# Optimization experiments

Measured on AMD Instinct MI355X. Metric: run time of the kernel, lower is better.

The kernel has to match this reference:

```python
import jax, jax.numpy as jnp
import numpy as np

B, S, D_IN, D_OUT = 4, 2048, 4096, 4096


def setup_inputs() -> dict:
    key = jax.random.key(0)
    k_x, k_w, k_s, k_b = jax.random.split(key, 4)
    x = jax.random.normal(k_x, (B, S, D_IN), dtype=jnp.float32)
    # simulated int8 compressed weight, values in [-128, 127]
    weight_int8 = jax.random.randint(k_w, (D_OUT, D_IN), 0, 255, dtype=jnp.int32) - 128
    # per-output-row dequant scale (positive)
    scale = jax.random.uniform(k_s, (D_OUT,), dtype=jnp.float32) * 0.01 + 1e-4
    bias = jax.random.normal(k_b, (D_OUT,), dtype=jnp.float32)
    return {"x": x, "weight_int8": weight_int8, "scale": scale, "bias": bias}


def reference(x, weight_int8, scale, bias):
    # dequantize: int8 -> fp, per-row scale, reshape to (out, in)
    weight_fp = weight_int8.astype(x.dtype) * scale[:, None]  # [D_OUT, D_IN]
    # F.linear: x @ W^T + b
    out = jnp.einsum("bsd,od->bso", x, weight_fp) + bias
    return out
```

## Files before the change

### kernel.cpp

```cpp
#include <hip/hip_runtime.h>


#define BM 256
#define BN 256
#define BKB 128

constexpr int Mdim = 8192;
constexpr int Ndim = 4096;
constexpr int Kdim = 4096;
constexpr int KT = Kdim / BKB;

typedef __attribute__((ext_vector_type(4)))  int   int32x4;
typedef __attribute__((ext_vector_type(16))) int   int32x16;
typedef __attribute__((ext_vector_type(8)))  short short8;
typedef __attribute__((ext_vector_type(4)))  float f32x4;
typedef unsigned short ushort_t;

__device__ __forceinline__ unsigned short f2bf(float f) {
    union { float f; unsigned u; } v; v.f = f;
    unsigned r = v.u + 0x7FFFu + ((v.u >> 16) & 1u);
    return (unsigned short)(r >> 16);
}

__device__ __forceinline__ void gload_lds16(const void* g, void* l) {
    __builtin_amdgcn_global_load_lds(
        (const __attribute__((address_space(1))) void*)g,
        (__attribute__((address_space(3))) void*)l, 16, 0, 0);
}

#define BARRIER() __builtin_amdgcn_s_barrier()
#define LGKM0()   asm volatile("s_waitcnt lgkmcnt(0)" ::: "memory")
#define WAITV0()  asm volatile("s_waitcnt vmcnt(0)" ::: "memory")
#define WAITV6()  asm volatile("s_waitcnt vmcnt(6)" ::: "memory")

#define MFMAQ(MH, NH) do {                                                   \
    __builtin_amdgcn_s_setprio(1);                                           \
    _Pragma("unroll") for (int mt = 0; mt < 2; ++mt)                         \
    _Pragma("unroll") for (int ks = 0; ks < 4; ++ks)                         \
        acc[(MH)*2+mt][NH] = __builtin_amdgcn_mfma_i32_32x32x32_i8(          \
            af[mt][ks], bf[NH][ks], acc[(MH)*2+mt][NH], 0, 0, 0);            \
    __builtin_amdgcn_s_setprio(0);                                           \
} while (0)


__global__ __launch_bounds__(256)
void quant_x_rowwise(const float* __restrict__ x, char* __restrict__ xq,
                     float* __restrict__ sx) {
    const int row = blockIdx.x;
    const float4* xr = reinterpret_cast<const float4*>(x + (size_t)row * Kdim);
    const int tid = threadIdx.x;
    float4 v[4];
    float am = 0.f;
    #pragma unroll
    for (int j = 0; j < 4; ++j) {
        v[j] = xr[tid + 256 * j];
        am = fmaxf(am, fmaxf(fmaxf(fabsf(v[j].x), fabsf(v[j].y)),
                             fmaxf(fabsf(v[j].z), fabsf(v[j].w))));
    }
    #pragma unroll
    for (int off = 32; off; off >>= 1)
        am = fmaxf(am, __shfl_xor(am, off, 64));
    __shared__ float red[4];
    if ((tid & 63) == 0) red[tid >> 6] = am;
    __syncthreads();
    am = fmaxf(fmaxf(red[0], red[1]), fmaxf(red[2], red[3]));
    am = fmaxf(am, 1e-30f);
    if (tid == 0) sx[row] = am / 127.f;
    const float inv = 127.f / am;
    int* outw = reinterpret_cast<int*>(xq + (size_t)row * Kdim);
    #pragma unroll
    for (int j = 0; j < 4; ++j) {
        const int q0 = (int)rintf(v[j].x * inv) & 255;
        const int q1 = (int)rintf(v[j].y * inv) & 255;
        const int q2 = (int)rintf(v[j].z * inv) & 255;
        const int q3 = (int)rintf(v[j].w * inv) & 255;
        outw[tid + 256 * j] = q0 | (q1 << 8) | (q2 << 16) | (q3 << 24);
    }
}

__global__ __launch_bounds__(256)
void pack_w_int8(const int* __restrict__ w, char* __restrict__ wq, int n4) {
    int idx = blockIdx.x * blockDim.x + threadIdx.x;
    const int stride = gridDim.x * blockDim.x;
    int* out = reinterpret_cast<int*>(wq);
    for (int i = idx; i < n4; i += stride) {
        const int4 a = reinterpret_cast<const int4*>(w)[i];
        out[i] = (a.x & 255) | ((a.y & 255) << 8) |
                 ((a.z & 255) << 16) | ((a.w & 255) << 24);
    }
}


__global__ __launch_bounds__(512, 2)
void gemm_i8_8phase(const char* __restrict__ A,
                    const char* __restrict__ B,
                    const float* __restrict__ scale,
                    const float* __restrict__ bias,
                    const float* __restrict__ sx,
                    float* __restrict__ Out)
{
    __shared__ __align__(16) char smem[2][4][16384];

    const int tid = threadIdx.x;
    int bid = blockIdx.x;
    bid = (bid & 7) * 64 + (bid >> 3);
    const int tn = bid & 15;
    const int tm = bid >> 4;
    const int brow = tm * BM;
    const int bcol = tn * BN;

    const int lane = tid & 63;
    const int w    = tid >> 6;
    const int wr   = w >> 2;
    const int wc   = w & 3;
    const int r32  = lane & 31;
    const int h    = lane >> 5;
    const size_t K1 = (size_t)Kdim;

    const int swzb = ((lane & 7) ^ (lane >> 3) ^ (w & 3)) << 4;
    const char* aStageSrc = A + (size_t)(brow + w * 8 + (lane >> 3)) * K1 + swzb;
    const char* bStageSrc = B + (size_t)(bcol + w * 8 + (lane >> 3)) * K1 + swzb;

    auto stageA = [&](int bufb, int hh, int tt) {
        const char* s = aStageSrc + (size_t)(hh * 128) * K1 + (size_t)tt * BKB;
        char* d = &smem[bufb][hh][w * 1024];
        gload_lds16(s, d);
        gload_lds16(s + 64 * K1, d + 8192);
    };
    auto stageB = [&](int bufb, int hh, int tt) {
        const char* s = bStageSrc + (size_t)(hh * 128) * K1 + (size_t)tt * BKB;
        char* d = &smem[bufb][2 + hh][w * 1024];
        gload_lds16(s, d);
        gload_lds16(s + 64 * K1, d + 8192);
    };

    const char* aBase[2] = { &smem[0][wr][0] + r32 * 128,
                             &smem[1][wr][0] + r32 * 128 };
    const char* bBase[2] = { &smem[0][2 + (wc >> 1)][0] + ((wc & 1) * 64 + r32) * 128,
                             &smem[1][2 + (wc >> 1)][0] + ((wc & 1) * 64 + r32) * 128 };
    const int frx = ((r32 & 7) ^ (r32 >> 3)) << 4;
    int colb[4];
    #pragma unroll
    for (int ks = 0; ks < 4; ++ks) colb[ks] = (ks * 32 + h * 16) ^ frx;

    int32x16 acc[4][2] = {};
    int32x4 af[2][4], bf[2][4];

    auto ldA = [&](const char* base, int MH) {
        #pragma unroll
        for (int mt = 0; mt < 2; ++mt) {
            const char* p = base + ((MH) * 2 + mt) * 4096;
            #pragma unroll
            for (int ks = 0; ks < 4; ++ks)
                af[mt][ks] = *reinterpret_cast<const int32x4*>(p + colb[ks]);
        }
    };
    auto ldB = [&](const char* base) {
        #pragma unroll
        for (int nt = 0; nt < 2; ++nt) {
            const char* p = base + nt * 4096;
            #pragma unroll
            for (int ks = 0; ks < 4; ++ks)
                bf[nt][ks] = *reinterpret_cast<const int32x4*>(p + colb[ks]);
        }
    };

    stageB(0, 0, 0); stageB(0, 1, 0); stageA(0, 0, 0); stageA(0, 1, 0);
    stageB(1, 0, 1); stageB(1, 1, 1); stageA(1, 0, 1);
    WAITV6();
    BARRIER();

    for (int i = 0; i < KT / 2 - 1; ++i) {
        const int t = 2 * i;

        ldB(bBase[0]); ldA(aBase[0], 0);
        stageA(1, 1, t + 1);
        BARRIER(); LGKM0();
        MFMAQ(0, 0);
        BARRIER();
        stageB(0, 0, t + 2);
        BARRIER(); LGKM0();
        MFMAQ(0, 1);
        BARRIER();
        ldA(aBase[0], 1);
        stageB(0, 1, t + 2);
        BARRIER(); LGKM0();
        MFMAQ(1, 0);
        BARRIER();
        stageA(0, 0, t + 2);
        BARRIER(); LGKM0();
        MFMAQ(1, 1);
        WAITV6();
        BARRIER();
        ldB(bBase[1]); ldA(aBase[1], 0);
        stageA(0, 1, t + 2);
        BARRIER(); LGKM0();
        MFMAQ(0, 0);
        BARRIER();
        stageB(1, 0, t + 3);
        BARRIER(); LGKM0();
        MFMAQ(0, 1);
        BARRIER();
        ldA(aBase[1], 1);
        stageB(1, 1, t + 3);
        BARRIER(); LGKM0();
        MFMAQ(1, 0);
        BARRIER();
        stageA(1, 0, t + 3);
        BARRIER(); LGKM0();
        MFMAQ(1, 1);
        WAITV6();
        BARRIER();
    }

    {
        ldB(bBase[0]); ldA(aBase[0], 0);
        stageA(1, 1, KT - 1);
        BARRIER(); LGKM0();
        MFMAQ(0, 0);
        BARRIER();
        MFMAQ(0, 1);
        BARRIER();
        ldA(aBase[0], 1);
        BARRIER(); LGKM0();
        MFMAQ(1, 0);
        BARRIER();
        MFMAQ(1, 1);
        WAITV0();
        BARRIER();
        ldB(bBase[1]); ldA(aBase[1], 0);
        BARRIER(); LGKM0();
        MFMAQ(0, 0);
        MFMAQ(0, 1);
        ldA(aBase[1], 1);
        LGKM0();
        MFMAQ(1, 0);
        MFMAQ(1, 1);
    }

    #pragma unroll
    for (int nt = 0; nt < 2; ++nt) {
        const int col = bcol + wc * 64 + nt * 32 + r32;
        const float sc = scale[col];
        const float bi = bias[col];
        #pragma unroll
        for (int mt = 0; mt < 4; ++mt) {
            const int rb = brow + wr * 128 + mt * 32 + 4 * h;
            #pragma unroll
            for (int q = 0; q < 4; ++q) {
                const int r4 = rb + 8 * q;
                #pragma unroll
                for (int r = 0; r < 4; ++r) {
                    const float sxr = sx[r4 + r];
                    Out[(size_t)(r4 + r) * Ndim + col] =
                        (float)acc[mt][nt][q * 4 + r] * (sc * sxr) + bi;
                }
            }
        }
    }
}


__device__ __forceinline__ int swz_fb(int row, int colbyte) {
    return row * 128 + (colbyte ^ ((row & 7) << 4));
}

__global__ __launch_bounds__(256)
void compressed_linear_fb(const float* __restrict__ X,
                          const int*   __restrict__ W,
                          const float* __restrict__ scale,
                          const float* __restrict__ bias,
                          float* __restrict__ Out)
{
    __shared__ __align__(16) ushort_t lA[128 * 64];
    __shared__ __align__(16) ushort_t lB[128 * 64];
    const int tid = threadIdx.x;
    const int bid = blockIdx.x;
    const int tn = bid & 31, tm = bid >> 5;
    const int brow = tm * 128, bcol = tn * 128;
    const int r0 = tid >> 3, c0 = tid & 7;
    float4 aPre[4][2]; int4 bPre[4][2];
    const int lane = tid & 63, w = tid >> 6;
    const int wr = w >> 1, wc = w & 1, fr = lane & 15, fq = lane >> 4;
    f32x4 acc[4][4] = {};

    auto loadTiles = [&](int t) {
        const int k0 = t * 64;
        #pragma unroll
        for (int i = 0; i < 4; i++) {
            const int row = r0 + 32 * i;
            const float4* pa = reinterpret_cast<const float4*>(X + (size_t)(brow + row) * Kdim + k0 + c0 * 8);
            aPre[i][0] = pa[0]; aPre[i][1] = pa[1];
            const int4* pb = reinterpret_cast<const int4*>(W + (size_t)(bcol + row) * Kdim + k0 + c0 * 8);
            bPre[i][0] = pb[0]; bPre[i][1] = pb[1];
        }
    };
    auto writeLDS = [&]() {
        #pragma unroll
        for (int i = 0; i < 4; i++) {
            const int row = r0 + 32 * i;
            const int off = swz_fb(row, c0 * 16);
            short8 va, vb;
            va[0] = (short)f2bf(aPre[i][0].x); va[1] = (short)f2bf(aPre[i][0].y);
            va[2] = (short)f2bf(aPre[i][0].z); va[3] = (short)f2bf(aPre[i][0].w);
            va[4] = (short)f2bf(aPre[i][1].x); va[5] = (short)f2bf(aPre[i][1].y);
            va[6] = (short)f2bf(aPre[i][1].z); va[7] = (short)f2bf(aPre[i][1].w);
            vb[0] = (short)f2bf((float)bPre[i][0].x); vb[1] = (short)f2bf((float)bPre[i][0].y);
            vb[2] = (short)f2bf((float)bPre[i][0].z); vb[3] = (short)f2bf((float)bPre[i][0].w);
            vb[4] = (short)f2bf((float)bPre[i][1].x); vb[5] = (short)f2bf((float)bPre[i][1].y);
            vb[6] = (short)f2bf((float)bPre[i][1].z); vb[7] = (short)f2bf((float)bPre[i][1].w);
            *reinterpret_cast<short8*>(reinterpret_cast<char*>(lA) + off) = va;
            *reinterpret_cast<short8*>(reinterpret_cast<char*>(lB) + off) = vb;
        }
    };

    loadTiles(0);
    for (int t = 0; t < Kdim / 64; t++) {
        writeLDS();
        __syncthreads();
        if (t + 1 < Kdim / 64) loadTiles(t + 1);
        #pragma unroll
        for (int kk = 0; kk < 2; kk++) {
            short8 afv[4], bfv[4];
            const int cb = kk * 64 + fq * 16;
            #pragma unroll
            for (int m = 0; m < 4; m++) {
                const int row = wr * 64 + m * 16 + fr;
                afv[m] = *reinterpret_cast<const short8*>(reinterpret_cast<const char*>(lA) + swz_fb(row, cb));
            }
            #pragma unroll
            for (int n = 0; n < 4; n++) {
                const int row = wc * 64 + n * 16 + fr;
                bfv[n] = *reinterpret_cast<const short8*>(reinterpret_cast<const char*>(lB) + swz_fb(row, cb));
            }
            #pragma unroll
            for (int m = 0; m < 4; m++)
                #pragma unroll
                for (int n = 0; n < 4; n++)
                    acc[m][n] = __builtin_amdgcn_mfma_f32_16x16x32_bf16(afv[m], bfv[n], acc[m][n], 0, 0, 0);
        }
        __syncthreads();
    }
    #pragma unroll
    for (int n = 0; n < 4; n++) {
        const int col = bcol + wc * 64 + n * 16 + fr;
        const float sc = scale[col];
        const float bi = bias[col];
        #pragma unroll
        for (int m = 0; m < 4; m++) {
            const int rbase = brow + wr * 64 + m * 16 + fq * 4;
            #pragma unroll
            for (int j = 0; j < 4; j++)
                Out[(size_t)(rbase + j) * Ndim + col] = acc[m][n][j] * sc + bi;
        }
    }
}


extern "C" void kernel_launch(void* const* d_in, const int* in_sizes, int n_in,
                              void* d_out, int out_size, void* d_ws, size_t ws_size,
                              hipStream_t stream) {
    const float* x     = (const float*)d_in[0];
    const int*   w8    = (const int*)d_in[1];
    const float* scale = (const float*)d_in[2];
    const float* bias  = (const float*)d_in[3];
    float* out = (float*)d_out;

    const size_t xq_bytes = (size_t)Mdim * Kdim;
    const size_t wq_bytes = (size_t)Ndim * Kdim;
    const size_t sx_bytes = (size_t)Mdim * sizeof(float);

    if (ws_size >= xq_bytes + wq_bytes + sx_bytes) {
        char*  xq = (char*)d_ws;
        char*  wq = (char*)d_ws + xq_bytes;
        float* sx = (float*)((char*)d_ws + xq_bytes + wq_bytes);
        quant_x_rowwise<<<Mdim, 256, 0, stream>>>(x, xq, sx);
        pack_w_int8<<<2048, 256, 0, stream>>>(w8, wq, (Ndim * Kdim) / 4);
        dim3 grid((Mdim / BM) * (Ndim / BN));
        gemm_i8_8phase<<<grid, dim3(512), 0, stream>>>(xq, wq, scale, bias, sx, out);
    } else {
        dim3 grid((Mdim / 128) * (Ndim / 128));
        compressed_linear_fb<<<grid, dim3(256), 0, stream>>>(x, w8, scale, bias, out);
    }
}
```

Before: 194.2 us.

## Shrink int8 GEMM tile to 128x128 with 4 waves and restructured staging

Replaces the 256x256 tile, 8-wave int8 MFMA GEMM with a 128x128 tile, 4-wave kernel. Each K-step is staged into LDS as a whole tile per buffer instead of in half-tile pieces, and the interleaving of LDS fragment loads and global-to-LDS stages within the phase loop is reworked. Smaller tiles give more blocks and less LDS per block, which may raise occupancy. In exchange, arithmetic intensity per block drops and global and L2 traffic for A and B roughly doubles.

```diff
diff --git a/kernel.cpp b/kernel.cpp
--- a/kernel.cpp
+++ b/kernel.cpp
@@ -1,8 +1,8 @@
 #include <hip/hip_runtime.h>
 
 
-#define BM 256
-#define BN 256
+#define BM 128
+#define BN 128
 #define BKB 128
 
 constexpr int Mdim = 8192;
@@ -31,14 +31,13 @@
 #define BARRIER() __builtin_amdgcn_s_barrier()
 #define LGKM0()   asm volatile("s_waitcnt lgkmcnt(0)" ::: "memory")
 #define WAITV0()  asm volatile("s_waitcnt vmcnt(0)" ::: "memory")
-#define WAITV6()  asm volatile("s_waitcnt vmcnt(6)" ::: "memory")
-
-#define MFMAQ(MH, NH) do {                                                   \
+#define WAITV8()  asm volatile("s_waitcnt vmcnt(8)" ::: "memory")
+
+#define MFMAQ(MT, NT) do {                                                   \
     __builtin_amdgcn_s_setprio(1);                                           \
-    _Pragma("unroll") for (int mt = 0; mt < 2; ++mt)                         \
     _Pragma("unroll") for (int ks = 0; ks < 4; ++ks)                         \
-        acc[(MH)*2+mt][NH] = __builtin_amdgcn_mfma_i32_32x32x32_i8(          \
-            af[mt][ks], bf[NH][ks], acc[(MH)*2+mt][NH], 0, 0, 0);            \
+        acc[MT][NT] = __builtin_amdgcn_mfma_i32_32x32x32_i8(                 \
+            af[MT][ks], bf[NT][ks], acc[MT][NT], 0, 0, 0);                   \
     __builtin_amdgcn_s_setprio(0);                                           \
 } while (0)
 
@@ -91,28 +90,28 @@
 }
 
 
-__global__ __launch_bounds__(512, 2)
-void gemm_i8_8phase(const char* __restrict__ A,
-                    const char* __restrict__ B,
-                    const float* __restrict__ scale,
-                    const float* __restrict__ bias,
-                    const float* __restrict__ sx,
-                    float* __restrict__ Out)
+__global__ __launch_bounds__(256, 2)
+void gemm_i8_128(const char* __restrict__ A,
+                 const char* __restrict__ B,
+                 const float* __restrict__ scale,
+                 const float* __restrict__ bias,
+                 const float* __restrict__ sx,
+                 float* __restrict__ Out)
 {
-    __shared__ __align__(16) char smem[2][4][16384];
+    __shared__ __align__(16) char smem[2][2][16384];
 
     const int tid = threadIdx.x;
     int bid = blockIdx.x;
-    bid = (bid & 7) * 64 + (bid >> 3);
-    const int tn = bid & 15;
-    const int tm = bid >> 4;
+    bid = (bid & 7) * 256 + (bid >> 3);
+    const int tn = bid & 31;
+    const int tm = bid >> 5;
     const int brow = tm * BM;
     const int bcol = tn * BN;
 
     const int lane = tid & 63;
     const int w    = tid >> 6;
-    const int wr   = w >> 2;
-    const int wc   = w & 3;
+    const int wr   = w >> 1;
+    const int wc   = w & 1;
     const int r32  = lane & 31;
     const int h    = lane >> 5;
     const size_t K1 = (size_t)Kdim;
@@ -121,104 +120,97 @@
     const char* aStageSrc = A + (size_t)(brow + w * 8 + (lane >> 3)) * K1 + swzb;
     const char* bStageSrc = B + (size_t)(bcol + w * 8 + (lane >> 3)) * K1 + swzb;
 
-    auto stageA = [&](int bufb, int hh, int tt) {
-        const char* s = aStageSrc + (size_t)(hh * 128) * K1 + (size_t)tt * BKB;
-        char* d = &smem[bufb][hh][w * 1024];
-        gload_lds16(s, d);
-        gload_lds16(s + 64 * K1, d + 8192);
-    };
-    auto stageB = [&](int bufb, int hh, int tt) {
-        const char* s = bStageSrc + (size_t)(hh * 128) * K1 + (size_t)tt * BKB;
-        char* d = &smem[bufb][2 + hh][w * 1024];
-        gload_lds16(s, d);
-        gload_lds16(s + 64 * K1, d + 8192);
-    };
-
-    const char* aBase[2] = { &smem[0][wr][0] + r32 * 128,
-                             &smem[1][wr][0] + r32 * 128 };
-    const char* bBase[2] = { &smem[0][2 + (wc >> 1)][0] + ((wc & 1) * 64 + r32) * 128,
-                             &smem[1][2 + (wc >> 1)][0] + ((wc & 1) * 64 + r32) * 128 };
+    auto stageA = [&](int bufb, int tt) {
+        const char* s = aStageSrc + (size_t)tt * BKB;
+        char* d = &smem[bufb][0][w * 1024];
+        #pragma unroll
+        for (int i = 0; i < 4; ++i)
+            gload_lds16(s + (size_t)(32 * i) * K1, d + i * 4096);
+    };
+    auto stageB = [&](int bufb, int tt) {
+        const char* s = bStageSrc + (size_t)tt * BKB;
+        char* d = &smem[bufb][1][w * 1024];
+        #pragma unroll
+        for (int i = 0; i < 4; ++i)
+            gload_lds16(s + (size_t)(32 * i) * K1, d + i * 4096);
+    };
+
+    const char* aBase[2] = { &smem[0][0][0] + (wr * 64 + r32) * 128,
+                             &smem[1][0][0] + (wr * 64 + r32) * 128 };
+    const char* bBase[2] = { &smem[0][1][0] + (wc * 64 + r32) * 128,
+                             &smem[1][1][0] + (wc * 64 + r32) * 128 };
     const int frx = ((r32 & 7) ^ (r32 >> 3)) << 4;
     int colb[4];
     #pragma unroll
     for (int ks = 0; ks < 4; ++ks) colb[ks] = (ks * 32 + h * 16) ^ frx;
 
-    int32x16 acc[4][2] = {};
+    int32x16 acc[2][2] = {};
     int32x4 af[2][4], bf[2][4];
 
-    auto ldA = [&](const char* base, int MH) {
-        #pragma unroll
-        for (int mt = 0; mt < 2; ++mt) {
-            const char* p = base + ((MH) * 2 + mt) * 4096;
-            #pragma unroll
-            for (int ks = 0; ks < 4; ++ks)
-                af[mt][ks] = *reinterpret_cast<const int32x4*>(p + colb[ks]);
-        }
-    };
-    auto ldB = [&](const char* base) {
-        #pragma unroll
-        for (int nt = 0; nt < 2; ++nt) {
-            const char* p = base + nt * 4096;
-            #pragma unroll
-            for (int ks = 0; ks < 4; ++ks)
-                bf[nt][ks] = *reinterpret_cast<const int32x4*>(p + colb[ks]);
-        }
-    };
-
-    stageB(0, 0, 0); stageB(0, 1, 0); stageA(0, 0, 0); stageA(0, 1, 0);
-    stageB(1, 0, 1); stageB(1, 1, 1); stageA(1, 0, 1);
-    WAITV6();
+    auto ldA = [&](const char* base, int mt) {
+        #pragma unroll
+        for (int ks = 0; ks < 4; ++ks)
+            af[mt][ks] = *reinterpret_cast<const int32x4*>(base + mt * 4096 + colb[ks]);
+    };
+    auto ldB = [&](const char* base, int nt) {
+        #pragma unroll
+        for (int ks = 0; ks < 4; ++ks)
+            bf[nt][ks] = *reinterpret_cast<const int32x4*>(base + nt * 4096 + colb[ks]);
+    };
+
+    stageB(0, 0); stageA(0, 0);
+    stageB(1, 1); stageA(1, 1);
+    WAITV8();
     BARRIER();
 
     for (int i = 0; i < KT / 2 - 1; ++i) {
         const int t = 2 * i;
 
-        ldB(bBase[0]); ldA(aBase[0], 0);
-        stageA(1, 1, t + 1);
+        ldA(aBase[0], 0); ldB(bBase[0], 0);
         BARRIER(); LGKM0();
         MFMAQ(0, 0);
         BARRIER();
-        stageB(0, 0, t + 2);
+        ldB(bBase[0], 1);
         BARRIER(); LGKM0();
         MFMAQ(0, 1);
         BARRIER();
         ldA(aBase[0], 1);
-        stageB(0, 1, t + 2);
+        stageB(0, t + 2);
         BARRIER(); LGKM0();
         MFMAQ(1, 0);
         BARRIER();
-        stageA(0, 0, t + 2);
+        stageA(0, t + 2);
         BARRIER(); LGKM0();
         MFMAQ(1, 1);
-        WAITV6();
-        BARRIER();
-        ldB(bBase[1]); ldA(aBase[1], 0);
-        stageA(0, 1, t + 2);
+        WAITV8();
+        BARRIER();
+        ldA(aBase[1], 0); ldB(bBase[1], 0);
         BARRIER(); LGKM0();
         MFMAQ(0, 0);
         BARRIER();
-        stageB(1, 0, t + 3);
+        ldB(bBase[1], 1);
         BARRIER(); LGKM0();
         MFMAQ(0, 1);
         BARRIER();
         ldA(aBase[1], 1);
-        stageB(1, 1, t + 3);
+        stageB(1, t + 3);
         BARRIER(); LGKM0();
         MFMAQ(1, 0);
         BARRIER();
-        stageA(1, 0, t + 3);
+        stageA(1, t + 3);
         BARRIER(); LGKM0();
         MFMAQ(1, 1);
-        WAITV6();
+        WAITV8();
         BARRIER();
     }
 
     {
-        ldB(bBase[0]); ldA(aBase[0], 0);
-        stageA(1, 1, KT - 1);
+        ldA(aBase[0], 0); ldB(bBase[0], 0);
         BARRIER(); LGKM0();
         MFMAQ(0, 0);
         BARRIER();
+        ldB(bBase[0], 1);
+        BARRIER(); LGKM0();
         MFMAQ(0, 1);
         BARRIER();
         ldA(aBase[0], 1);
@@ -228,9 +220,11 @@
         MFMAQ(1, 1);
         WAITV0();
         BARRIER();
-        ldB(bBase[1]); ldA(aBase[1], 0);
-        BARRIER(); LGKM0();
+        ldA(aBase[1], 0); ldB(bBase[1], 0);
+        LGKM0();
         MFMAQ(0, 0);
+        ldB(bBase[1], 1);
+        LGKM0();
         MFMAQ(0, 1);
         ldA(aBase[1], 1);
         LGKM0();
@@ -244,8 +238,8 @@
         const float sc = scale[col];
         const float bi = bias[col];
         #pragma unroll
-        for (int mt = 0; mt < 4; ++mt) {
-            const int rb = brow + wr * 128 + mt * 32 + 4 * h;
+        for (int mt = 0; mt < 2; ++mt) {
+            const int rb = brow + wr * 64 + mt * 32 + 4 * h;
             #pragma unroll
             for (int q = 0; q < 4; ++q) {
                 const int r4 = rb + 8 * q;
@@ -377,7 +371,7 @@
         quant_x_rowwise<<<Mdim, 256, 0, stream>>>(x, xq, sx);
         pack_w_int8<<<2048, 256, 0, stream>>>(w8, wq, (Ndim * Kdim) / 4);
         dim3 grid((Mdim / BM) * (Ndim / BN));
-        gemm_i8_8phase<<<grid, dim3(512), 0, stream>>>(xq, wq, scale, bias, sx, out);
+        gemm_i8_128<<<grid, dim3(256), 0, stream>>>(xq, wq, scale, bias, sx, out);
     } else {
         dim3 grid((Mdim / 128) * (Ndim / 128));
         compressed_linear_fb<<<grid, dim3(256), 0, stream>>>(x, w8, scale, bias, out);
```

Result: slower. 223.9 us (+15.3%).

## Replace eight-phase interleaved GEMM schedule with two-cluster flat pipeline

Applied to the files above, without the earlier changes.

Restructures the int8 MFMA main loop. The old schedule split each K-tile into four small MFMA quadrants, each wrapped in barriers and explicit LDS waits; the new one runs two larger MFMA clusters per K-tile, covering both N halves at once. All global-to-LDS staging for a future tile is issued between the two clusters, and the vmcnt threshold changes to match the new issue order. The aim is to cut barrier and waitcnt overhead and give the MFMA units longer uninterrupted runs. The cost is coarser interleaving of memory traffic with compute, and more in-flight loads bunched together.

```diff
diff --git a/kernel.cpp b/kernel.cpp
--- a/kernel.cpp
+++ b/kernel.cpp
@@ -29,16 +29,16 @@
 }
 
 #define BARRIER() __builtin_amdgcn_s_barrier()
-#define LGKM0()   asm volatile("s_waitcnt lgkmcnt(0)" ::: "memory")
 #define WAITV0()  asm volatile("s_waitcnt vmcnt(0)" ::: "memory")
-#define WAITV6()  asm volatile("s_waitcnt vmcnt(6)" ::: "memory")
-
-#define MFMAQ(MH, NH) do {                                                   \
+#define WAITV4()  asm volatile("s_waitcnt vmcnt(4)" ::: "memory")
+
+#define CLUSTER(MBASE) do {                                                  \
     __builtin_amdgcn_s_setprio(1);                                           \
     _Pragma("unroll") for (int mt = 0; mt < 2; ++mt)                         \
+    _Pragma("unroll") for (int nt = 0; nt < 2; ++nt)                         \
     _Pragma("unroll") for (int ks = 0; ks < 4; ++ks)                         \
-        acc[(MH)*2+mt][NH] = __builtin_amdgcn_mfma_i32_32x32x32_i8(          \
-            af[mt][ks], bf[NH][ks], acc[(MH)*2+mt][NH], 0, 0, 0);            \
+        acc[(MBASE)+mt][nt] = __builtin_amdgcn_mfma_i32_32x32x32_i8(         \
+            af[mt][ks], bf[nt][ks], acc[(MBASE)+mt][nt], 0, 0, 0);           \
     __builtin_amdgcn_s_setprio(0);                                           \
 } while (0)
 
@@ -92,12 +92,12 @@
 
 
 __global__ __launch_bounds__(512, 2)
-void gemm_i8_8phase(const char* __restrict__ A,
-                    const char* __restrict__ B,
-                    const float* __restrict__ scale,
-                    const float* __restrict__ bias,
-                    const float* __restrict__ sx,
-                    float* __restrict__ Out)
+void gemm_i8_flat(const char* __restrict__ A,
+                  const char* __restrict__ B,
+                  const float* __restrict__ scale,
+                  const float* __restrict__ bias,
+                  const float* __restrict__ sx,
+                  float* __restrict__ Out)
 {
     __shared__ __align__(16) char smem[2][4][16384];
 
@@ -165,77 +165,52 @@
         }
     };
 
-    stageB(0, 0, 0); stageB(0, 1, 0); stageA(0, 0, 0); stageA(0, 1, 0);
-    stageB(1, 0, 1); stageB(1, 1, 1); stageA(1, 0, 1);
-    WAITV6();
+    stageA(0, 0, 0); stageA(0, 1, 0);
+    stageB(0, 0, 0); stageB(0, 1, 0);
+    stageB(1, 0, 1); stageB(1, 1, 1);
+    WAITV4();
     BARRIER();
 
     for (int i = 0; i < KT / 2 - 1; ++i) {
         const int t = 2 * i;
 
         ldB(bBase[0]); ldA(aBase[0], 0);
-        stageA(1, 1, t + 1);
-        BARRIER(); LGKM0();
-        MFMAQ(0, 0);
-        BARRIER();
-        stageB(0, 0, t + 2);
-        BARRIER(); LGKM0();
-        MFMAQ(0, 1);
-        BARRIER();
+        BARRIER();
+        CLUSTER(0);
         ldA(aBase[0], 1);
-        stageB(0, 1, t + 2);
-        BARRIER(); LGKM0();
-        MFMAQ(1, 0);
-        BARRIER();
-        stageA(0, 0, t + 2);
-        BARRIER(); LGKM0();
-        MFMAQ(1, 1);
-        WAITV6();
-        BARRIER();
+        stageA(1, 0, t + 1); stageA(1, 1, t + 1);
+        stageB(0, 0, t + 2); stageB(0, 1, t + 2);
+        CLUSTER(2);
+        WAITV4();
+        BARRIER();
+
         ldB(bBase[1]); ldA(aBase[1], 0);
-        stageA(0, 1, t + 2);
-        BARRIER(); LGKM0();
-        MFMAQ(0, 0);
-        BARRIER();
-        stageB(1, 0, t + 3);
-        BARRIER(); LGKM0();
-        MFMAQ(0, 1);
-        BARRIER();
+        BARRIER();
+        CLUSTER(0);
         ldA(aBase[1], 1);
-        stageB(1, 1, t + 3);
-        BARRIER(); LGKM0();
-        MFMAQ(1, 0);
-        BARRIER();
-        stageA(1, 0, t + 3);
-        BARRIER(); LGKM0();
-        MFMAQ(1, 1);
-        WAITV6();
+        stageA(0, 0, t + 2); stageA(0, 1, t + 2);
+        stageB(1, 0, t + 3); stageB(1, 1, t + 3);
+        CLUSTER(2);
+        WAITV4();
         BARRIER();
     }
 
     {
         ldB(bBase[0]); ldA(aBase[0], 0);
-        stageA(1, 1, KT - 1);
-        BARRIER(); LGKM0();
-        MFMAQ(0, 0);
-        BARRIER();
-        MFMAQ(0, 1);
-        BARRIER();
+        BARRIER();
+        CLUSTER(0);
         ldA(aBase[0], 1);
-        BARRIER(); LGKM0();
-        MFMAQ(1, 0);
-        BARRIER();
-        MFMAQ(1, 1);
+        stageA(1, 0, KT - 1); stageA(1, 1, KT - 1);
+        CLUSTER(2);
         WAITV0();
         BARRIER();
+    }
+    {
         ldB(bBase[1]); ldA(aBase[1], 0);
-        BARRIER(); LGKM0();
-        MFMAQ(0, 0);
-        MFMAQ(0, 1);
+        BARRIER();
+        CLUSTER(0);
         ldA(aBase[1], 1);
-        LGKM0();
-        MFMAQ(1, 0);
-        MFMAQ(1, 1);
+        CLUSTER(2);
     }
 
     #pragma unroll
@@ -377,7 +352,7 @@
         quant_x_rowwise<<<Mdim, 256, 0, stream>>>(x, xq, sx);
         pack_w_int8<<<2048, 256, 0, stream>>>(w8, wq, (Ndim * Kdim) / 4);
         dim3 grid((Mdim / BM) * (Ndim / BN));
-        gemm_i8_8phase<<<grid, dim3(512), 0, stream>>>(xq, wq, scale, bias, sx, out);
+        gemm_i8_flat<<<grid, dim3(512), 0, stream>>>(xq, wq, scale, bias, sx, out);
     } else {
         dim3 grid((Mdim / 128) * (Ndim / 128));
         compressed_linear_fb<<<grid, dim3(256), 0, stream>>>(x, w8, scale, bias, out);
```

New measurement: 194.5 us. No clear change (+0.2%).

## Software-pipeline LDS fragment loads with MFMA using split A register buffers

Applied to the files above, without the earlier changes.

Restructures the int8 GEMM main loop so LDS reads of the next fragments (A high half, next-buffer B and A low half) are issued while MFMAs on the current fragments execute. A fragments are split into separate Lo/Hi register sets, and the loop drops to one barrier per phase instead of two. The vmcnt wait is tightened so stage arrival is checked earlier. The extra live fragment registers raise register pressure at two blocks per CU, and the reordered barriers need the LDS buffer reuse to stay race-free.

```diff
diff --git a/kernel.cpp b/kernel.cpp
--- a/kernel.cpp
+++ b/kernel.cpp
@@ -31,14 +31,15 @@
 #define BARRIER() __builtin_amdgcn_s_barrier()
 #define LGKM0()   asm volatile("s_waitcnt lgkmcnt(0)" ::: "memory")
 #define WAITV0()  asm volatile("s_waitcnt vmcnt(0)" ::: "memory")
+#define WAITV4()  asm volatile("s_waitcnt vmcnt(4)" ::: "memory")
 #define WAITV6()  asm volatile("s_waitcnt vmcnt(6)" ::: "memory")
 
-#define MFMAQ(MH, NH) do {                                                   \
+#define MFMAC(AF, MB, NH) do {                                               \
     __builtin_amdgcn_s_setprio(1);                                           \
     _Pragma("unroll") for (int mt = 0; mt < 2; ++mt)                         \
     _Pragma("unroll") for (int ks = 0; ks < 4; ++ks)                         \
-        acc[(MH)*2+mt][NH] = __builtin_amdgcn_mfma_i32_32x32x32_i8(          \
-            af[mt][ks], bf[NH][ks], acc[(MH)*2+mt][NH], 0, 0, 0);            \
+        acc[(MB)+mt][NH] = __builtin_amdgcn_mfma_i32_32x32x32_i8(            \
+            AF[mt][ks], bf[NH][ks], acc[(MB)+mt][NH], 0, 0, 0);              \
     __builtin_amdgcn_s_setprio(0);                                           \
 } while (0)
 
@@ -92,12 +93,12 @@
 
 
 __global__ __launch_bounds__(512, 2)
-void gemm_i8_8phase(const char* __restrict__ A,
-                    const char* __restrict__ B,
-                    const float* __restrict__ scale,
-                    const float* __restrict__ bias,
-                    const float* __restrict__ sx,
-                    float* __restrict__ Out)
+void gemm_i8_pl(const char* __restrict__ A,
+                const char* __restrict__ B,
+                const float* __restrict__ scale,
+                const float* __restrict__ bias,
+                const float* __restrict__ sx,
+                float* __restrict__ Out)
 {
     __shared__ __align__(16) char smem[2][4][16384];
 
@@ -144,98 +145,98 @@
     for (int ks = 0; ks < 4; ++ks) colb[ks] = (ks * 32 + h * 16) ^ frx;
 
     int32x16 acc[4][2] = {};
-    int32x4 af[2][4], bf[2][4];
-
-    auto ldA = [&](const char* base, int MH) {
-        #pragma unroll
-        for (int mt = 0; mt < 2; ++mt) {
-            const char* p = base + ((MH) * 2 + mt) * 4096;
+    int32x4 afLo[2][4], afHi[2][4], bf[2][4];
+
+    auto ldB = [&](const char* base) {
+        #pragma unroll
+        for (int nt = 0; nt < 2; ++nt)
             #pragma unroll
             for (int ks = 0; ks < 4; ++ks)
-                af[mt][ks] = *reinterpret_cast<const int32x4*>(p + colb[ks]);
-        }
-    };
-    auto ldB = [&](const char* base) {
-        #pragma unroll
-        for (int nt = 0; nt < 2; ++nt) {
-            const char* p = base + nt * 4096;
+                bf[nt][ks] = *reinterpret_cast<const int32x4*>(base + nt * 4096 + colb[ks]);
+    };
+    auto ldALo = [&](const char* base) {
+        #pragma unroll
+        for (int mt = 0; mt < 2; ++mt)
             #pragma unroll
             for (int ks = 0; ks < 4; ++ks)
-                bf[nt][ks] = *reinterpret_cast<const int32x4*>(p + colb[ks]);
-        }
+                afLo[mt][ks] = *reinterpret_cast<const int32x4*>(base + mt * 4096 + colb[ks]);
+    };
+    auto ldAHi = [&](const char* base) {
+        #pragma unroll
+        for (int mt = 0; mt < 2; ++mt)
+            #pragma unroll
+            for (int ks = 0; ks < 4; ++ks)
+                afHi[mt][ks] = *reinterpret_cast<const int32x4*>(base + (2 + mt) * 4096 + colb[ks]);
     };
 
     stageB(0, 0, 0); stageB(0, 1, 0); stageA(0, 0, 0); stageA(0, 1, 0);
     stageB(1, 0, 1); stageB(1, 1, 1); stageA(1, 0, 1);
     WAITV6();
     BARRIER();
+    ldB(bBase[0]);
+    ldALo(aBase[0]);
+    BARRIER();
 
     for (int i = 0; i < KT / 2 - 1; ++i) {
         const int t = 2 * i;
 
-        ldB(bBase[0]); ldA(aBase[0], 0);
+        MFMAC(afLo, 0, 0);
+        ldAHi(aBase[0]);
         stageA(1, 1, t + 1);
-        BARRIER(); LGKM0();
-        MFMAQ(0, 0);
-        BARRIER();
+        LGKM0();
+        BARRIER();
+        MFMAC(afLo, 0, 1);
         stageB(0, 0, t + 2);
-        BARRIER(); LGKM0();
-        MFMAQ(0, 1);
-        BARRIER();
-        ldA(aBase[0], 1);
+        BARRIER();
+        MFMAC(afHi, 2, 0);
         stageB(0, 1, t + 2);
-        BARRIER(); LGKM0();
-        MFMAQ(1, 0);
-        BARRIER();
+        LGKM0();
+        WAITV4();
+        BARRIER();
+        MFMAC(afHi, 2, 1);
+        ldB(bBase[1]);
+        ldALo(aBase[1]);
         stageA(0, 0, t + 2);
-        BARRIER(); LGKM0();
-        MFMAQ(1, 1);
-        WAITV6();
-        BARRIER();
-        ldB(bBase[1]); ldA(aBase[1], 0);
+        BARRIER();
+        MFMAC(afLo, 0, 0);
+        ldAHi(aBase[1]);
         stageA(0, 1, t + 2);
-        BARRIER(); LGKM0();
-        MFMAQ(0, 0);
-        BARRIER();
+        LGKM0();
+        BARRIER();
+        MFMAC(afLo, 0, 1);
         stageB(1, 0, t + 3);
-        BARRIER(); LGKM0();
-        MFMAQ(0, 1);
-        BARRIER();
-        ldA(aBase[1], 1);
+        BARRIER();
+        MFMAC(afHi, 2, 0);
         stageB(1, 1, t + 3);
-        BARRIER(); LGKM0();
-        MFMAQ(1, 0);
-        BARRIER();
+        LGKM0();
+        WAITV4();
+        BARRIER();
+        MFMAC(afHi, 2, 1);
+        ldB(bBase[0]);
+        ldALo(aBase[0]);
         stageA(1, 0, t + 3);
-        BARRIER(); LGKM0();
-        MFMAQ(1, 1);
-        WAITV6();
         BARRIER();
     }
 
     {
-        ldB(bBase[0]); ldA(aBase[0], 0);
+        MFMAC(afLo, 0, 0);
+        ldAHi(aBase[0]);
         stageA(1, 1, KT - 1);
-        BARRIER(); LGKM0();
-        MFMAQ(0, 0);
-        BARRIER();
-        MFMAQ(0, 1);
-        BARRIER();
-        ldA(aBase[0], 1);
-        BARRIER(); LGKM0();
-        MFMAQ(1, 0);
-        BARRIER();
-        MFMAQ(1, 1);
+        LGKM0();
+        BARRIER();
+        MFMAC(afLo, 0, 1);
+        BARRIER();
+        MFMAC(afHi, 2, 0);
         WAITV0();
         BARRIER();
-        ldB(bBase[1]); ldA(aBase[1], 0);
-        BARRIER(); LGKM0();
-        MFMAQ(0, 0);
-        MFMAQ(0, 1);
-        ldA(aBase[1], 1);
-        LGKM0();
-        MFMAQ(1, 0);
-        MFMAQ(1, 1);
+        MFMAC(afHi, 2, 1);
+        ldB(bBase[1]);
+        ldALo(aBase[1]);
+        MFMAC(afLo, 0, 0);
+        ldAHi(aBase[1]);
+        MFMAC(afLo, 0, 1);
+        MFMAC(afHi, 2, 0);
+        MFMAC(afHi, 2, 1);
     }
 
     #pragma unroll
@@ -377,7 +378,7 @@
         quant_x_rowwise<<<Mdim, 256, 0, stream>>>(x, xq, sx);
         pack_w_int8<<<2048, 256, 0, stream>>>(w8, wq, (Ndim * Kdim) / 4);
         dim3 grid((Mdim / BM) * (Ndim / BN));
-        gemm_i8_8phase<<<grid, dim3(512), 0, stream>>>(xq, wq, scale, bias, sx, out);
+        gemm_i8_pl<<<grid, dim3(512), 0, stream>>>(xq, wq, scale, bias, sx, out);
     } else {
         dim3 grid((Mdim / 128) * (Ndim / 128));
         compressed_linear_fb<<<grid, dim3(256), 0, stream>>>(x, w8, scale, bias, out);
```

Measured after the change: 196.3 us. No clear change (+1.1%).
